# Kernel optimization log

Hardware: AMD Instinct MI355X
Metric: run time of the kernel (lower is better)

Reference implementation:

```python
import jax, jax.numpy as jnp
import numpy as np

N_NODES = 100000
N_EDGES = 1600000
IN_DIM, HID_DIM, OUT_DIM = 2, 128, 128


def setup_inputs() -> dict:
    key = jax.random.key(0)
    ks = jax.random.split(key, 8)
    x = jax.random.normal(ks[0], (N_NODES, IN_DIM), dtype=jnp.float32)
    edge_index = jax.random.randint(ks[1], (2, N_EDGES), 0, N_NODES, dtype=jnp.int64)
    s = 0.1
    return {
        "x": x,
        "edge_index": edge_index,
        # SAGEConv layer 1: lin_l (on aggregated neighbors, with bias) + lin_r (root)
        "W_l1": jax.random.normal(ks[2], (IN_DIM, HID_DIM), dtype=jnp.float32) * s,
        "W_r1": jax.random.normal(ks[3], (IN_DIM, HID_DIM), dtype=jnp.float32) * s,
        "b1": jnp.zeros((HID_DIM,), dtype=jnp.float32),
        # SAGEConv layer 2
        "W_l2": jax.random.normal(ks[4], (HID_DIM, OUT_DIM), dtype=jnp.float32) * s,
        "W_r2": jax.random.normal(ks[5], (HID_DIM, OUT_DIM), dtype=jnp.float32) * s,
        "b2": jnp.zeros((OUT_DIM,), dtype=jnp.float32),
    }


def _sage_conv(h, src, dst, Wl, Wr, b):
    # PyG SAGEConv (aggr='mean'): out_i = Wl @ mean_{j in N(i)} h_j + Wr @ h_i + b
    msg = h[src]                                              # [E, D] gather
    agg = jax.ops.segment_sum(msg, dst, num_segments=N_NODES)  # [N, D] scatter-add
    deg = jax.ops.segment_sum(jnp.ones_like(dst, dtype=h.dtype), dst,
                              num_segments=N_NODES)
    agg = agg / jnp.maximum(deg, 1.0)[:, None]                # mean aggregation
    return agg @ Wl + h @ Wr + b


def reference(x, edge_index, W_l1, W_r1, b1, W_l2, W_r2, b2):
    src, dst = edge_index[0], edge_index[1]  # messages flow src -> dst
    h = _sage_conv(x, src, dst, W_l1, W_r1, b1)
    h = jax.nn.relu(h)  # dropout p=0.1 is identity in eval mode
    out = _sage_conv(h, src, dst, W_l2, W_r2, b2)
    return out
```

## Files before the change

### kernel.cpp

```cpp
#include <hip/hip_runtime.h>


using f32x4 = __attribute__((ext_vector_type(4))) float;
using s16x8 = __attribute__((ext_vector_type(8))) short;

__device__ __forceinline__ unsigned short f32_to_bf16(float f) {
  unsigned int u = __float_as_uint(f);
  u += 0x7fffu + ((u >> 16) & 1u);
  return (unsigned short)(u >> 16);
}
__device__ __forceinline__ float bf16lo(unsigned int p) { return __uint_as_float(p << 16); }
__device__ __forceinline__ float bf16hi(unsigned int p) { return __uint_as_float(p & 0xffff0000u); }

#define EDGE_TILE 4096

__global__ __launch_bounds__(256) void k_bhist(const int* __restrict__ ei, int* __restrict__ bcnt,
                                               int E, int nb) {
  __shared__ int h[1024];
  int t = threadIdx.x;
  for (int i = t; i < nb; i += 256) h[i] = 0;
  __syncthreads();
  int tbeg = blockIdx.x * EDGE_TILE;
  int tend = min(tbeg + EDGE_TILE, E);
  const int* dstp = ei + E;
  for (int i = tbeg + t; i < tend; i += 256) atomicAdd(&h[dstp[i] >> 7], 1);
  __syncthreads();
  for (int i = t; i < nb; i += 256) if (h[i]) atomicAdd(&bcnt[i], h[i]);
}

__global__ __launch_bounds__(1024) void k_bscan(const int* __restrict__ bcnt, int* __restrict__ bbase,
                                                int* __restrict__ bcur, int nb, int E) {
  __shared__ int sm[2][1024];
  int t = threadIdx.x;
  int v0 = (t < nb) ? bcnt[t] : 0;
  sm[0][t] = v0;
  __syncthreads();
  int src = 0;
  for (int st = 1; st < 1024; st <<= 1) {
    int v = sm[src][t];
    if (t >= st) v += sm[src][t - st];
    sm[src ^ 1][t] = v; __syncthreads(); src ^= 1;
  }
  int ex = sm[src][t] - v0;
  if (t < nb) { bbase[t] = ex; bcur[t] = ex; }
  if (t == 0) bbase[nb] = E;
}

__global__ __launch_bounds__(256) void k_bscatter(const int* __restrict__ ei, int* __restrict__ bcur,
                                                  uint2* __restrict__ ebuf, int E, int nb) {
  __shared__ int h[1024];
  __shared__ int base[1024];
  int t = threadIdx.x;
  for (int i = t; i < nb; i += 256) h[i] = 0;
  __syncthreads();
  int tbeg = blockIdx.x * EDGE_TILE;
  int tend = min(tbeg + EDGE_TILE, E);
  const int* srcp = ei;
  const int* dstp = ei + E;
  for (int i = tbeg + t; i < tend; i += 256) atomicAdd(&h[dstp[i] >> 7], 1);
  __syncthreads();
  for (int i = t; i < nb; i += 256) {
    int c = h[i];
    base[i] = c ? atomicAdd(&bcur[i], c) : 0;
    h[i] = 0;
  }
  __syncthreads();
  for (int i = tbeg + t; i < tend; i += 256) {
    int d = dstp[i];
    int b = d >> 7;
    int r = atomicAdd(&h[b], 1);
    ebuf[base[b] + r] = make_uint2((unsigned)srcp[i], (unsigned)d);
  }
}

__global__ __launch_bounds__(256) void k_bucket_csr(const uint2* __restrict__ ebuf,
                                                    const int* __restrict__ bbase,
                                                    int* __restrict__ offs, int* __restrict__ csr,
                                                    int N, int nb) {
  __shared__ int deg[128];
  __shared__ int loff[128];
  __shared__ int cur[128];
  int b = blockIdx.x;
  int t = threadIdx.x;
  int lo = bbase[b], hi = bbase[b + 1];
  if (t < 128) deg[t] = 0;
  __syncthreads();
  for (int i = lo + t; i < hi; i += 256) atomicAdd(&deg[ebuf[i].y & 127], 1);
  __syncthreads();
  if (t < 128) loff[t] = deg[t];
  __syncthreads();
  for (int st = 1; st < 128; st <<= 1) {
    int v = 0;
    if (t < 128 && t >= st) v = loff[t - st];
    __syncthreads();
    if (t < 128) loff[t] += v;
    __syncthreads();
  }
  if (t < 128) {
    int ex = loff[t] - deg[t];
    cur[t] = ex;
    int node = b * 128 + t;
    if (node < N) offs[node] = lo + ex;
  }
  if (b == nb - 1 && t == 0) offs[N] = hi;
  __syncthreads();
  for (int i = lo + t; i < hi; i += 256) {
    uint2 e = ebuf[i];
    int r = atomicAdd(&cur[e.y & 127], 1);
    csr[lo + r] = (int)e.x;
  }
}

__global__ __launch_bounds__(256) void k_agg1(const int* __restrict__ offs, const int* __restrict__ csr,
                                              const float* __restrict__ x, float* __restrict__ agg1, int n) {
  int node = blockIdx.x * 256 + threadIdx.x;
  if (node >= n) return;
  int beg = offs[node], end = offs[node + 1];
  float s0 = 0.f, s1 = 0.f;
  const float2* x2 = (const float2*)x;
  for (int e = beg; e < end; ++e) {
    int s = csr[e];
    float2 v = x2[s];
    s0 += v.x; s1 += v.y;
  }
  agg1[2 * node] = s0; agg1[2 * node + 1] = s1;
}

__global__ __launch_bounds__(256) void k_layer1(const float* __restrict__ x, const float* __restrict__ agg1,
                                                const int* __restrict__ offs,
                                                const float* __restrict__ Wl, const float* __restrict__ Wr,
                                                const float* __restrict__ b1,
                                                unsigned int* __restrict__ h16, int n) {
  int gid = blockIdx.x * 256 + threadIdx.x;
  int node = gid >> 6;
  if (node >= n) return;
  int c = (gid & 63) * 2;
  int deg = offs[node + 1] - offs[node];
  float sc = 1.0f / (float)max(deg, 1);
  float a0 = agg1[2 * node] * sc, a1 = agg1[2 * node + 1] * sc;
  float x0 = x[2 * node], x1 = x[2 * node + 1];
  float r0 = fmaf(a0, Wl[c],     fmaf(a1, Wl[128 + c],     fmaf(x0, Wr[c],     fmaf(x1, Wr[128 + c],     b1[c]))));
  float r1 = fmaf(a0, Wl[c + 1], fmaf(a1, Wl[128 + c + 1], fmaf(x0, Wr[c + 1], fmaf(x1, Wr[128 + c + 1], b1[c + 1]))));
  r0 = r0 > 0.f ? r0 : 0.f;
  r1 = r1 > 0.f ? r1 : 0.f;
  unsigned int packed = (unsigned int)f32_to_bf16(r0) | ((unsigned int)f32_to_bf16(r1) << 16);
  h16[(size_t)node * 64 + (gid & 63)] = packed;
}

__global__ __launch_bounds__(256) void k_prepw(const float* __restrict__ Wl2, const float* __restrict__ Wr2,
                                               unsigned short* __restrict__ wt) {
  int tid = blockIdx.x * 256 + threadIdx.x;
  if (tid >= 128 * 256) return;
  int c = tid >> 8, k = tid & 255;
  float v = (k < 128) ? Wl2[k * 128 + c] : Wr2[(k - 128) * 128 + c];
  wt[tid] = f32_to_bf16(v);
}

__global__ __launch_bounds__(256) void k_agg2(const int* __restrict__ offs, const int* __restrict__ csr,
                                              const unsigned short* __restrict__ h16,
                                              unsigned int* __restrict__ a16, int n) {
  int node = blockIdx.x * 4 + (threadIdx.x >> 6);
  if (node >= n) return;
  int lane = threadIdx.x & 63;
  int g  = lane >> 4;
  int cb = lane & 15;
  int beg = offs[node], end = offs[node + 1];
  float acc[8];
#pragma unroll
  for (int j = 0; j < 8; ++j) acc[j] = 0.f;
  for (int e = beg; e < end; e += 4) {
    int idx = e + g;
    int cidx = idx < end ? idx : end - 1;
    float w = idx < end ? 1.f : 0.f;
    int s = csr[cidx];
    const uint4* p = (const uint4*)(h16 + (size_t)s * 128 + cb * 8);
    uint4 v = *p;
    acc[0] = fmaf(w, bf16lo(v.x), acc[0]); acc[1] = fmaf(w, bf16hi(v.x), acc[1]);
    acc[2] = fmaf(w, bf16lo(v.y), acc[2]); acc[3] = fmaf(w, bf16hi(v.y), acc[3]);
    acc[4] = fmaf(w, bf16lo(v.z), acc[4]); acc[5] = fmaf(w, bf16hi(v.z), acc[5]);
    acc[6] = fmaf(w, bf16lo(v.w), acc[6]); acc[7] = fmaf(w, bf16hi(v.w), acc[7]);
  }
#pragma unroll
  for (int j = 0; j < 8; ++j) {
    acc[j] += __shfl_xor(acc[j], 16, 64);
    acc[j] += __shfl_xor(acc[j], 32, 64);
  }
  if (g == 0) {
    int deg = end - beg;
    float scale = 1.0f / (float)max(deg, 1);
    uint4 o;
    o.x = (unsigned int)f32_to_bf16(acc[0] * scale) | ((unsigned int)f32_to_bf16(acc[1] * scale) << 16);
    o.y = (unsigned int)f32_to_bf16(acc[2] * scale) | ((unsigned int)f32_to_bf16(acc[3] * scale) << 16);
    o.z = (unsigned int)f32_to_bf16(acc[4] * scale) | ((unsigned int)f32_to_bf16(acc[5] * scale) << 16);
    o.w = (unsigned int)f32_to_bf16(acc[6] * scale) | ((unsigned int)f32_to_bf16(acc[7] * scale) << 16);
    *(uint4*)(a16 + (size_t)node * 64 + cb * 4) = o;
  }
}

__global__ __launch_bounds__(256) void k_gemm(const unsigned short* __restrict__ a16,
                                              const unsigned short* __restrict__ h16,
                                              const unsigned short* __restrict__ wt,
                                              const float* __restrict__ b2,
                                              float* __restrict__ out, int nrows) {
  __shared__ unsigned short bs[64 * 264];
  int half = blockIdx.x & 1;
  int tg   = blockIdx.x >> 1;

#pragma unroll
  for (int i = 0; i < 8; ++i) {
    int c = threadIdx.x + i * 256;
    int row = c >> 5, off = c & 31;
    *(uint4*)(bs + row * 264 + off * 8) =
        *(const uint4*)(wt + ((size_t)(half * 64 + row)) * 256 + off * 8);
  }
  __syncthreads();

  int wv   = threadIdx.x >> 6;
  int lane = threadIdx.x & 63;
  int m16 = lane & 15, quad = lane >> 4;
  int tile = tg * 4 + wv;
  if (tile * 16 >= nrows) return;

  int r  = tile * 16 + m16;
  int rc = r < nrows ? r : nrows - 1;
  const unsigned short* arow = a16 + (size_t)rc * 128 + quad * 8;
  const unsigned short* hrow = h16 + (size_t)rc * 128 + quad * 8;

  s16x8 afrag[8];
#pragma unroll
  for (int c4 = 0; c4 < 4; ++c4) {
    afrag[c4]     = *(const s16x8*)(arow + c4 * 32);
    afrag[4 + c4] = *(const s16x8*)(hrow + c4 * 32);
  }

  f32x4 acc[4];
#pragma unroll
  for (int t = 0; t < 4; ++t) acc[t] = (f32x4){0.f, 0.f, 0.f, 0.f};

  const unsigned short* bbase = bs + m16 * 264 + quad * 8;
#pragma unroll
  for (int ch = 0; ch < 8; ++ch) {
#pragma unroll
    for (int t = 0; t < 4; ++t) {
      s16x8 bf = *(const s16x8*)(bbase + t * 16 * 264 + ch * 32);
      acc[t] = __builtin_amdgcn_mfma_f32_16x16x32_bf16(afrag[ch], bf, acc[t], 0, 0, 0);
    }
  }

#pragma unroll
  for (int t = 0; t < 4; ++t) {
    int col = half * 64 + t * 16 + m16;
    float bias = b2[col];
#pragma unroll
    for (int i = 0; i < 4; ++i) {
      int row = tile * 16 + quad * 4 + i;
      if (row < nrows) out[(size_t)row * 128 + col] = acc[t][i] + bias;
    }
  }
}

extern "C" void kernel_launch(void* const* d_in, const int* in_sizes, int n_in,
                              void* d_out, int out_size, void* d_ws, size_t ws_size,
                              hipStream_t stream) {
  const float* x    = (const float*)d_in[0];
  const int*   ei   = (const int*)d_in[1];
  const float* Wl1  = (const float*)d_in[2];
  const float* Wr1  = (const float*)d_in[3];
  const float* b1   = (const float*)d_in[4];
  const float* Wl2  = (const float*)d_in[5];
  const float* Wr2  = (const float*)d_in[6];
  const float* b2   = (const float*)d_in[7];
  float* out = (float*)d_out;

  const int N = in_sizes[0] / 2;
  const int E = in_sizes[1] / 2;
  const int nb = (N + 127) >> 7;

  char* p = (char*)d_ws;
  auto take = [&](size_t bytes) { char* r = p; p += (bytes + 255) & ~(size_t)255; return r; };
  int* bcnt            = (int*)take(1024 * 4);
  int* bbase           = (int*)take(1025 * 4);
  int* bcur            = (int*)take(1024 * 4);
  int* offs            = (int*)take((size_t)(N + 1) * 4);
  int* csr             = (int*)take((size_t)E * 4);
  uint2* ebuf          = (uint2*)take((size_t)E * 8);
  float* agg1          = (float*)take((size_t)N * 2 * 4);
  unsigned short* h16  = (unsigned short*)take((size_t)N * 128 * 2);
  unsigned short* a16  = (unsigned short*)take((size_t)N * 128 * 2);
  unsigned short* wt   = (unsigned short*)take((size_t)128 * 256 * 2);

  const int nblk_e = (E + EDGE_TILE - 1) / EDGE_TILE;
  const int ntiles = (N + 15) / 16;

  hipMemsetAsync(bcnt, 0, 1024 * 4, stream);

  k_bhist     <<<nblk_e, 256, 0, stream>>>(ei, bcnt, E, nb);
  k_bscan     <<<1, 1024, 0, stream>>>(bcnt, bbase, bcur, nb, E);
  k_bscatter  <<<nblk_e, 256, 0, stream>>>(ei, bcur, ebuf, E, nb);
  k_bucket_csr<<<nb, 256, 0, stream>>>(ebuf, bbase, offs, csr, N, nb);
  k_agg1      <<<(N + 255) / 256, 256, 0, stream>>>(offs, csr, x, agg1, N);
  k_layer1    <<<((size_t)N * 64 + 255) / 256, 256, 0, stream>>>(x, agg1, offs, Wl1, Wr1, b1,
                                                                 (unsigned int*)h16, N);
  k_prepw     <<<(128 * 256) / 256, 256, 0, stream>>>(Wl2, Wr2, wt);
  k_agg2      <<<(N + 3) / 4, 256, 0, stream>>>(offs, csr, h16, (unsigned int*)a16, N);
  k_gemm      <<<((ntiles + 3) / 4) * 2, 256, 0, stream>>>(a16, h16, wt, b2, out, N);
}
```

Measured before the change: 277.5 us.

## Gather layer-2 neighbor features in FP8 and pack edge buffer into 32 bits

Layer 1 now also writes an FP8 copy of the hidden activations, and the layer-2 neighbor aggregation gathers from that copy instead of the BF16 one. Each gathered row is halved in size, so each wave covers 8 edges per iteration with 16 channels per lane. Separately, the bucketed edge buffer packs the source index and the low 7 bits of the destination into one 32-bit word, which halves the scatter/CSR traffic. The FP8 (e4m3) path adds quantization error to the mean aggregation and an extra FP8 write in layer 1. The packing only holds while source indices fit in 25 bits.

```diff
diff --git a/kernel.cpp b/kernel.cpp
--- a/kernel.cpp
+++ b/kernel.cpp
@@ -2,6 +2,7 @@
 
 
 using f32x4 = __attribute__((ext_vector_type(4))) float;
+using f32x2 = __attribute__((ext_vector_type(2))) float;
 using s16x8 = __attribute__((ext_vector_type(8))) short;
 
 __device__ __forceinline__ unsigned short f32_to_bf16(float f) {
@@ -9,8 +10,6 @@
   u += 0x7fffu + ((u >> 16) & 1u);
   return (unsigned short)(u >> 16);
 }
-__device__ __forceinline__ float bf16lo(unsigned int p) { return __uint_as_float(p << 16); }
-__device__ __forceinline__ float bf16hi(unsigned int p) { return __uint_as_float(p & 0xffff0000u); }
 
 #define EDGE_TILE 4096
 
@@ -47,7 +46,7 @@
 }
 
 __global__ __launch_bounds__(256) void k_bscatter(const int* __restrict__ ei, int* __restrict__ bcur,
-                                                  uint2* __restrict__ ebuf, int E, int nb) {
+                                                  unsigned int* __restrict__ ebuf, int E, int nb) {
   __shared__ int h[1024];
   __shared__ int base[1024];
   int t = threadIdx.x;
@@ -69,11 +68,11 @@
     int d = dstp[i];
     int b = d >> 7;
     int r = atomicAdd(&h[b], 1);
-    ebuf[base[b] + r] = make_uint2((unsigned)srcp[i], (unsigned)d);
-  }
-}
-
-__global__ __launch_bounds__(256) void k_bucket_csr(const uint2* __restrict__ ebuf,
+    ebuf[base[b] + r] = ((unsigned)srcp[i] << 7) | (unsigned)(d & 127);
+  }
+}
+
+__global__ __launch_bounds__(256) void k_bucket_csr(const unsigned int* __restrict__ ebuf,
                                                     const int* __restrict__ bbase,
                                                     int* __restrict__ offs, int* __restrict__ csr,
                                                     int N, int nb) {
@@ -85,7 +84,7 @@
   int lo = bbase[b], hi = bbase[b + 1];
   if (t < 128) deg[t] = 0;
   __syncthreads();
-  for (int i = lo + t; i < hi; i += 256) atomicAdd(&deg[ebuf[i].y & 127], 1);
+  for (int i = lo + t; i < hi; i += 256) atomicAdd(&deg[ebuf[i] & 127], 1);
   __syncthreads();
   if (t < 128) loff[t] = deg[t];
   __syncthreads();
@@ -105,9 +104,9 @@
   if (b == nb - 1 && t == 0) offs[N] = hi;
   __syncthreads();
   for (int i = lo + t; i < hi; i += 256) {
-    uint2 e = ebuf[i];
-    int r = atomicAdd(&cur[e.y & 127], 1);
-    csr[lo + r] = (int)e.x;
+    unsigned int e = ebuf[i];
+    int r = atomicAdd(&cur[e & 127], 1);
+    csr[lo + r] = (int)(e >> 7);
   }
 }
 
@@ -130,7 +129,8 @@
                                                 const int* __restrict__ offs,
                                                 const float* __restrict__ Wl, const float* __restrict__ Wr,
                                                 const float* __restrict__ b1,
-                                                unsigned int* __restrict__ h16, int n) {
+                                                unsigned int* __restrict__ h16,
+                                                unsigned short* __restrict__ h8, int n) {
   int gid = blockIdx.x * 256 + threadIdx.x;
   int node = gid >> 6;
   if (node >= n) return;
@@ -145,6 +145,8 @@
   r1 = r1 > 0.f ? r1 : 0.f;
   unsigned int packed = (unsigned int)f32_to_bf16(r0) | ((unsigned int)f32_to_bf16(r1) << 16);
   h16[(size_t)node * 64 + (gid & 63)] = packed;
+  unsigned int p8 = (unsigned int)__builtin_amdgcn_cvt_pk_fp8_f32(r0, r1, 0, false);
+  h8[(size_t)node * 64 + (gid & 63)] = (unsigned short)(p8 & 0xffffu);
 }
 
 __global__ __launch_bounds__(256) void k_prepw(const float* __restrict__ Wl2, const float* __restrict__ Wr2,
@@ -157,43 +159,50 @@
 }
 
 __global__ __launch_bounds__(256) void k_agg2(const int* __restrict__ offs, const int* __restrict__ csr,
-                                              const unsigned short* __restrict__ h16,
+                                              const unsigned char* __restrict__ h8,
                                               unsigned int* __restrict__ a16, int n) {
   int node = blockIdx.x * 4 + (threadIdx.x >> 6);
   if (node >= n) return;
   int lane = threadIdx.x & 63;
-  int g  = lane >> 4;
-  int cb = lane & 15;
+  int g  = lane >> 3;
+  int cb = lane & 7;
   int beg = offs[node], end = offs[node + 1];
-  float acc[8];
-#pragma unroll
-  for (int j = 0; j < 8; ++j) acc[j] = 0.f;
-  for (int e = beg; e < end; e += 4) {
+  float acc[16];
+#pragma unroll
+  for (int j = 0; j < 16; ++j) acc[j] = 0.f;
+  for (int e = beg; e < end; e += 8) {
     int idx = e + g;
     int cidx = idx < end ? idx : end - 1;
     float w = idx < end ? 1.f : 0.f;
     int s = csr[cidx];
-    const uint4* p = (const uint4*)(h16 + (size_t)s * 128 + cb * 8);
-    uint4 v = *p;
-    acc[0] = fmaf(w, bf16lo(v.x), acc[0]); acc[1] = fmaf(w, bf16hi(v.x), acc[1]);
-    acc[2] = fmaf(w, bf16lo(v.y), acc[2]); acc[3] = fmaf(w, bf16hi(v.y), acc[3]);
-    acc[4] = fmaf(w, bf16lo(v.z), acc[4]); acc[5] = fmaf(w, bf16hi(v.z), acc[5]);
-    acc[6] = fmaf(w, bf16lo(v.w), acc[6]); acc[7] = fmaf(w, bf16hi(v.w), acc[7]);
-  }
-#pragma unroll
-  for (int j = 0; j < 8; ++j) {
+    uint4 v = *(const uint4*)(h8 + (size_t)s * 128 + cb * 16);
+    f32x2 p;
+    p = __builtin_amdgcn_cvt_pk_f32_fp8((int)v.x, false); acc[0] = fmaf(w, p[0], acc[0]);  acc[1] = fmaf(w, p[1], acc[1]);
+    p = __builtin_amdgcn_cvt_pk_f32_fp8((int)v.x, true);  acc[2] = fmaf(w, p[0], acc[2]);  acc[3] = fmaf(w, p[1], acc[3]);
+    p = __builtin_amdgcn_cvt_pk_f32_fp8((int)v.y, false); acc[4] = fmaf(w, p[0], acc[4]);  acc[5] = fmaf(w, p[1], acc[5]);
+    p = __builtin_amdgcn_cvt_pk_f32_fp8((int)v.y, true);  acc[6] = fmaf(w, p[0], acc[6]);  acc[7] = fmaf(w, p[1], acc[7]);
+    p = __builtin_amdgcn_cvt_pk_f32_fp8((int)v.z, false); acc[8] = fmaf(w, p[0], acc[8]);  acc[9] = fmaf(w, p[1], acc[9]);
+    p = __builtin_amdgcn_cvt_pk_f32_fp8((int)v.z, true);  acc[10] = fmaf(w, p[0], acc[10]); acc[11] = fmaf(w, p[1], acc[11]);
+    p = __builtin_amdgcn_cvt_pk_f32_fp8((int)v.w, false); acc[12] = fmaf(w, p[0], acc[12]); acc[13] = fmaf(w, p[1], acc[13]);
+    p = __builtin_amdgcn_cvt_pk_f32_fp8((int)v.w, true);  acc[14] = fmaf(w, p[0], acc[14]); acc[15] = fmaf(w, p[1], acc[15]);
+  }
+#pragma unroll
+  for (int j = 0; j < 16; ++j) {
+    acc[j] += __shfl_xor(acc[j], 8, 64);
     acc[j] += __shfl_xor(acc[j], 16, 64);
     acc[j] += __shfl_xor(acc[j], 32, 64);
   }
   if (g == 0) {
     int deg = end - beg;
     float scale = 1.0f / (float)max(deg, 1);
-    uint4 o;
-    o.x = (unsigned int)f32_to_bf16(acc[0] * scale) | ((unsigned int)f32_to_bf16(acc[1] * scale) << 16);
-    o.y = (unsigned int)f32_to_bf16(acc[2] * scale) | ((unsigned int)f32_to_bf16(acc[3] * scale) << 16);
-    o.z = (unsigned int)f32_to_bf16(acc[4] * scale) | ((unsigned int)f32_to_bf16(acc[5] * scale) << 16);
-    o.w = (unsigned int)f32_to_bf16(acc[6] * scale) | ((unsigned int)f32_to_bf16(acc[7] * scale) << 16);
-    *(uint4*)(a16 + (size_t)node * 64 + cb * 4) = o;
+    unsigned int u[8];
+#pragma unroll
+    for (int k = 0; k < 8; ++k)
+      u[k] = (unsigned int)f32_to_bf16(acc[2 * k] * scale) |
+             ((unsigned int)f32_to_bf16(acc[2 * k + 1] * scale) << 16);
+    unsigned int* dst = a16 + (size_t)node * 64 + cb * 8;
+    *(uint4*)dst       = make_uint4(u[0], u[1], u[2], u[3]);
+    *(uint4*)(dst + 4) = make_uint4(u[4], u[5], u[6], u[7]);
   }
 }
 
@@ -283,10 +292,11 @@
   int* bcur            = (int*)take(1024 * 4);
   int* offs            = (int*)take((size_t)(N + 1) * 4);
   int* csr             = (int*)take((size_t)E * 4);
-  uint2* ebuf          = (uint2*)take((size_t)E * 8);
+  unsigned int* ebuf   = (unsigned int*)take((size_t)E * 4);
   float* agg1          = (float*)take((size_t)N * 2 * 4);
   unsigned short* h16  = (unsigned short*)take((size_t)N * 128 * 2);
   unsigned short* a16  = (unsigned short*)take((size_t)N * 128 * 2);
+  unsigned short* h8   = (unsigned short*)take((size_t)N * 128);
   unsigned short* wt   = (unsigned short*)take((size_t)128 * 256 * 2);
 
   const int nblk_e = (E + EDGE_TILE - 1) / EDGE_TILE;
@@ -300,8 +310,9 @@
   k_bucket_csr<<<nb, 256, 0, stream>>>(ebuf, bbase, offs, csr, N, nb);
   k_agg1      <<<(N + 255) / 256, 256, 0, stream>>>(offs, csr, x, agg1, N);
   k_layer1    <<<((size_t)N * 64 + 255) / 256, 256, 0, stream>>>(x, agg1, offs, Wl1, Wr1, b1,
-                                                                 (unsigned int*)h16, N);
+                                                                 (unsigned int*)h16, h8, N);
   k_prepw     <<<(128 * 256) / 256, 256, 0, stream>>>(Wl2, Wr2, wt);
-  k_agg2      <<<(N + 3) / 4, 256, 0, stream>>>(offs, csr, h16, (unsigned int*)a16, N);
+  k_agg2      <<<(N + 3) / 4, 256, 0, stream>>>(offs, csr, (const unsigned char*)h8,
+                                                (unsigned int*)a16, N);
   k_gemm      <<<((ntiles + 3) / 4) * 2, 256, 0, stream>>>(a16, h16, wt, b2, out, N);
 }
```

New measurement: 274.3 us. Within noise of the previous version (-1.1%).
